# Optimization experiments

Hardware: AMD Instinct MI355X
Metric: run time of the kernel (lower is better)

The kernel has to match this reference:

```python
import jax, jax.numpy as jnp
import numpy as np

N_NODES = 50000
N_EDGES = 800000
IN_DIM = 16
HID = 128
OUT_DIM = 1
N_LAYERS = 2


def setup_inputs() -> dict:
    key = jax.random.key(0)
    ks = jax.random.split(key, 16)
    s = 0.05
    inp = {
        "edge_feats": jax.random.normal(ks[0], (N_EDGES, IN_DIM), jnp.float32),
        "node_feats": jax.random.normal(ks[1], (N_NODES, 4), jnp.float32),
        "src": jax.random.randint(ks[2], (N_EDGES,), 0, N_NODES, jnp.int32),
        "dst": jax.random.randint(ks[3], (N_EDGES,), 0, N_NODES, jnp.int32),
        # edge_embedding (dead in original forward, kept for faithfulness)
        "W_eemb": jax.random.normal(ks[4], (IN_DIM, HID), jnp.float32) * s,
        "b_eemb": jnp.zeros((HID,), jnp.float32),
        # node_embedding: Linear(4, hidden)
        "W_nemb": jax.random.normal(ks[5], (4, HID), jnp.float32) * s,
        "b_nemb": jnp.zeros((HID,), jnp.float32),
        # stacked GraphConv weights [n_layers, H, H]
        "gnn_W": jax.random.normal(ks[6], (N_LAYERS, HID, HID), jnp.float32) * s,
        "gnn_b": jnp.zeros((N_LAYERS, HID), jnp.float32),
        # output MLP
        "out_W1": jax.random.normal(ks[7], (HID, HID), jnp.float32) * s,
        "out_b1": jnp.zeros((HID,), jnp.float32),
        "out_W2": jax.random.normal(ks[8], (HID, OUT_DIM), jnp.float32) * s,
        "out_b2": jnp.zeros((OUT_DIM,), jnp.float32),
    }
    return inp


def reference(edge_feats, node_feats, src, dst, W_eemb, b_eemb, W_nemb, b_nemb,
              gnn_W, gnn_b, out_W1, out_b1, out_W2, out_b2):
    ones = jnp.ones((src.shape[0],), jnp.float32)
    deg_out = jnp.clip(jax.ops.segment_sum(ones, src, num_segments=N_NODES), 1.0)
    deg_in = jnp.clip(jax.ops.segment_sum(ones, dst, num_segments=N_NODES), 1.0)
    norm_out = deg_out ** -0.5  # [N]
    norm_in = deg_in ** -0.5    # [N]

    # edge_embedding output is dead code in the original forward (overwritten)
    _h_e = edge_feats @ W_eemb + b_eemb

    h = node_feats @ W_nemb + b_nemb  # [N, H]
    for l in range(N_LAYERS):
        # DGL GraphConv norm='both': D_out^{-1/2} gather -> scatter-sum -> D_in^{-1/2} -> W, b
        hs = h * norm_out[:, None]
        agg = jax.ops.segment_sum(hs[src], dst, num_segments=N_NODES)  # [N, H]
        h = agg * norm_in[:, None]
        h = h @ gnn_W[l] + gnn_b[l]
        h = jax.nn.relu(h)

    edge_h = h[src] + h[dst]  # apply_edges UDF, [E, H]
    x = jax.nn.relu(edge_h @ out_W1 + out_b1)
    return x @ out_W2 + out_b2  # [E, OUT_DIM]
```

## Files before the change

### kernel.cpp

```cpp
#include <hip/hip_runtime.h>

#define N_NODES 50000
#define N_EDGES 800000
#define HID 128
#define AP2 132
#define NB 256
#define NPB 196

__device__ __forceinline__ unsigned pack2bf(float a, float b) {
  unsigned ua = __float_as_uint(a);
  ua += 0x7FFFu + ((ua >> 16) & 1u);
  unsigned ub = __float_as_uint(b);
  ub += 0x7FFFu + ((ub >> 16) & 1u);
  return (ua >> 16) | (ub & 0xFFFF0000u);
}
#define BFLO(u) __uint_as_float((u) << 16)
#define BFHI(u) __uint_as_float((u) & 0xFFFF0000u)


__global__ __launch_bounds__(256) void p1_hist_kernel(
    const int* __restrict__ src, const int* __restrict__ dst,
    int* __restrict__ bcnt_d, int* __restrict__ bcnt_s) {
  __shared__ int hd[NB], hs[NB];
  int t = threadIdx.x;
  hd[t] = 0; hs[t] = 0;
  __syncthreads();
  for (int e = blockIdx.x * 256 + t; e < N_EDGES; e += gridDim.x * 256) {
    atomicAdd(&hd[dst[e] / NPB], 1);
    atomicAdd(&hs[src[e] / NPB], 1);
  }
  __syncthreads();
  if (hd[t]) atomicAdd(&bcnt_d[t], hd[t]);
  if (hs[t]) atomicAdd(&bcnt_s[t], hs[t]);
}

__global__ void p2_scan_kernel(const int* __restrict__ bcnt_d, const int* __restrict__ bcnt_s,
                               int* __restrict__ bofs_d, int* __restrict__ bofs_s,
                               int* __restrict__ cur_d, int* __restrict__ cur_s) {
  __shared__ int s[NB];
  int t = threadIdx.x;
  int v = bcnt_d[t];
  s[t] = v;
  __syncthreads();
  for (int o = 1; o < NB; o <<= 1) {
    int x = (t >= o) ? s[t - o] : 0;
    __syncthreads();
    s[t] += x;
    __syncthreads();
  }
  int ofs = s[t] - v;
  bofs_d[t] = ofs; cur_d[t] = ofs;
  if (t == NB - 1) bofs_d[NB] = s[t];
  __syncthreads();
  v = bcnt_s[t];
  s[t] = v;
  __syncthreads();
  for (int o = 1; o < NB; o <<= 1) {
    int x = (t >= o) ? s[t - o] : 0;
    __syncthreads();
    s[t] += x;
    __syncthreads();
  }
  ofs = s[t] - v;
  bofs_s[t] = ofs; cur_s[t] = ofs;
  if (t == NB - 1) bofs_s[NB] = s[t];
}

__global__ __launch_bounds__(256) void p3_scatter_dst_kernel(
    const int* __restrict__ src, const int* __restrict__ dst,
    int* __restrict__ cur_d, int2* __restrict__ sdst) {
  __shared__ int bcnt[NB], bbase[NB];
  int t = threadIdx.x;
  int base = blockIdx.x * 2048;
  bcnt[t] = 0;
  __syncthreads();
  int myb[8], myr[8], mys[8], myp[8];
#pragma unroll
  for (int u = 0; u < 8; ++u) {
    int e = base + u * 256 + t;
    myb[u] = -1;
    if (e < N_EDGES) {
      int d = dst[e];
      int b = d / NPB;
      myb[u] = b;
      myr[u] = atomicAdd(&bcnt[b], 1);
      mys[u] = src[e];
      myp[u] = ((d - b * NPB) << 20) | e;
    }
  }
  __syncthreads();
  int c = bcnt[t];
  if (c) bbase[t] = atomicAdd(&cur_d[t], c);
  __syncthreads();
#pragma unroll
  for (int u = 0; u < 8; ++u) {
    if (myb[u] >= 0) sdst[bbase[myb[u]] + myr[u]] = make_int2(mys[u], myp[u]);
  }
}

__global__ __launch_bounds__(256) void p3_scatter_src_kernel(
    const int* __restrict__ src, int* __restrict__ cur_s, int* __restrict__ ssrc) {
  __shared__ int bcnt[NB], bbase[NB];
  int t = threadIdx.x;
  int base = blockIdx.x * 2048;
  bcnt[t] = 0;
  __syncthreads();
  int myb[8], myr[8], mys[8];
#pragma unroll
  for (int u = 0; u < 8; ++u) {
    int e = base + u * 256 + t;
    myb[u] = -1;
    if (e < N_EDGES) {
      int s = src[e];
      int b = s / NPB;
      myb[u] = b;
      myr[u] = atomicAdd(&bcnt[b], 1);
      mys[u] = s;
    }
  }
  __syncthreads();
  int c = bcnt[t];
  if (c) bbase[t] = atomicAdd(&cur_s[t], c);
  __syncthreads();
#pragma unroll
  for (int u = 0; u < 8; ++u) {
    if (myb[u] >= 0) ssrc[bbase[myb[u]] + myr[u]] = mys[u];
  }
}

__global__ __launch_bounds__(256) void p4_csr_kernel(
    const int2* __restrict__ sdst, const int* __restrict__ bofs_d,
    int* __restrict__ row_ofs, float* __restrict__ norm_in,
    int* __restrict__ csr_src, int* __restrict__ csr_eid) {
  __shared__ int hc[NB], sc[NB], cur[NB];
  int b = blockIdx.x, t = threadIdx.x;
  int base = bofs_d[b], cnt = bofs_d[b + 1] - base;
  hc[t] = 0;
  __syncthreads();
  for (int i = t; i < cnt; i += 256) atomicAdd(&hc[sdst[base + i].y >> 20], 1);
  __syncthreads();
  int v = hc[t];
  sc[t] = v;
  __syncthreads();
  for (int o = 1; o < NB; o <<= 1) {
    int x = (t >= o) ? sc[t - o] : 0;
    __syncthreads();
    sc[t] += x;
    __syncthreads();
  }
  int ofs = sc[t] - v;
  int node = b * NPB + t;
  if (t < NPB && node < N_NODES) {
    row_ofs[node] = base + ofs;
    norm_in[node] = rsqrtf((float)(v < 1 ? 1 : v));
  }
  cur[t] = base + ofs;
  if (b == 0 && t == 0) row_ofs[N_NODES] = N_EDGES;
  __syncthreads();
  for (int i = t; i < cnt; i += 256) {
    int2 e = sdst[base + i];
    int pos = atomicAdd(&cur[e.y >> 20], 1);
    csr_src[pos] = e.x;
    csr_eid[pos] = e.y & 0xFFFFF;
  }
}

__global__ __launch_bounds__(256) void p5_degout_kernel(
    const int* __restrict__ ssrc, const int* __restrict__ bofs_s,
    float* __restrict__ norm_out) {
  __shared__ int hc[NB];
  int b = blockIdx.x, t = threadIdx.x;
  int base = bofs_s[b], cnt = bofs_s[b + 1] - base;
  int lo = b * NPB;
  hc[t] = 0;
  __syncthreads();
  for (int i = t; i < cnt; i += 256) atomicAdd(&hc[ssrc[base + i] - lo], 1);
  __syncthreads();
  int node = lo + t;
  if (t < NPB && node < N_NODES) {
    int v = hc[t];
    norm_out[node] = rsqrtf((float)(v < 1 ? 1 : v));
  }
}


__global__ __launch_bounds__(256) void agg4_kernel(
    const float4* __restrict__ nf4, const float* __restrict__ no_,
    const int* __restrict__ csr_src, const int* __restrict__ row_ofs,
    float4* __restrict__ agg4, float* __restrict__ sno) {
  int wid = (blockIdx.x * blockDim.x + threadIdx.x) >> 6;
  int lane = threadIdx.x & 63;
  int g = lane >> 4, l = lane & 15;
  int v = wid * 4 + g;
  if (v >= N_NODES) return;
  int beg = row_ofs[v], end = row_ofs[v + 1];
  float ax = 0.f, ay = 0.f, az = 0.f, aw = 0.f, sn = 0.f;
  for (int i = beg + l; i < end; i += 16) {
    int s = csr_src[i];
    float w = no_[s];
    float4 n = nf4[s];
    ax += n.x * w; ay += n.y * w; az += n.z * w; aw += n.w * w;
    sn += w;
  }
#pragma unroll
  for (int o = 1; o < 16; o <<= 1) {
    ax += __shfl_xor(ax, o, 16);
    ay += __shfl_xor(ay, o, 16);
    az += __shfl_xor(az, o, 16);
    aw += __shfl_xor(aw, o, 16);
    sn += __shfl_xor(sn, o, 16);
  }
  if (l == 0) {
    agg4[v] = make_float4(ax, ay, az, aw);
    sno[v] = sn;
  }
}

__global__ __launch_bounds__(256) void gemm_l1_kernel(
    const float4* __restrict__ agg4, const float* __restrict__ sno,
    const float* __restrict__ ni_, const float* __restrict__ no_,
    const float* __restrict__ Wn, const float* __restrict__ bn,
    const float* __restrict__ W0, const float* __restrict__ b0,
    uint4* __restrict__ h1b, int nrows) {
  __shared__ float At[HID * 64];
  int t = threadIdx.x;
  int v0 = blockIdx.x * 64;
  {
    int r = t & 63, kg = t >> 6;
    int v = v0 + r;
    float4 a = make_float4(0.f, 0.f, 0.f, 0.f);
    float sn = 0.f, nin = 0.f;
    if (v < nrows) { a = agg4[v]; sn = sno[v]; nin = ni_[v]; }
    for (int kk = 0; kk < 32; ++kk) {
      int k = kg * 32 + kk;
      float val = (a.x * Wn[k] + a.y * Wn[HID + k] + a.z * Wn[2 * HID + k] +
                   a.w * Wn[3 * HID + k] + bn[k] * sn) * nin;
      At[k * 64 + r] = val;
    }
  }
  __syncthreads();
  int c0 = (t >> 4) * 8, r0 = (t & 15) * 4;
  float acc[4][8];
#pragma unroll
  for (int i = 0; i < 4; ++i)
#pragma unroll
    for (int j = 0; j < 8; ++j) acc[i][j] = 0.f;

#pragma unroll 4
  for (int k = 0; k < HID; ++k) {
    float4 av = *(const float4*)&At[k * 64 + r0];
    float4 w0v = *(const float4*)&W0[k * HID + c0];
    float4 w1v = *(const float4*)&W0[k * HID + c0 + 4];
    float ar[4] = {av.x, av.y, av.z, av.w};
    float wv[8] = {w0v.x, w0v.y, w0v.z, w0v.w, w1v.x, w1v.y, w1v.z, w1v.w};
#pragma unroll
    for (int i = 0; i < 4; ++i)
#pragma unroll
      for (int j = 0; j < 8; ++j) acc[i][j] += ar[i] * wv[j];
  }
  float bb[8];
  {
    float4 b0v = *(const float4*)&b0[c0];
    float4 b1v = *(const float4*)&b0[c0 + 4];
    bb[0] = b0v.x; bb[1] = b0v.y; bb[2] = b0v.z; bb[3] = b0v.w;
    bb[4] = b1v.x; bb[5] = b1v.y; bb[6] = b1v.z; bb[7] = b1v.w;
  }
#pragma unroll
  for (int i = 0; i < 4; ++i) {
    int v = v0 + r0 + i;
    if (v < nrows) {
      float nov = no_[v];
      float o[8];
#pragma unroll
      for (int j = 0; j < 8; ++j) o[j] = fmaxf(acc[i][j] + bb[j], 0.f) * nov;
      uint4 pk;
      pk.x = pack2bf(o[0], o[1]); pk.y = pack2bf(o[2], o[3]);
      pk.z = pack2bf(o[4], o[5]); pk.w = pack2bf(o[6], o[7]);
      h1b[(size_t)v * 16 + (c0 >> 3)] = pk;
    }
  }
}

__global__ __launch_bounds__(256) void aggregate_kernel(
    const uint4* __restrict__ hb, const int* __restrict__ row_ofs,
    const int* __restrict__ csr_src, const float* __restrict__ ni_,
    float* __restrict__ agg) {
  int v = (blockIdx.x * blockDim.x + threadIdx.x) >> 6;
  int lane = threadIdx.x & 63;
  if (v >= N_NODES) return;
  int beg = row_ofs[v], end = row_ofs[v + 1];
  int g = lane >> 4, l = lane & 15;
  float acc[8];
#pragma unroll
  for (int j = 0; j < 8; ++j) acc[j] = 0.f;
  for (int i = beg; i < end; i += 16) {
    int ii[4]; float mm[4]; int ss[4];
#pragma unroll
    for (int u = 0; u < 4; ++u) {
      ii[u] = i + 4 * u + g;
      bool q = ii[u] < end;
      mm[u] = q ? 1.f : 0.f;
      ss[u] = csr_src[q ? ii[u] : beg];
    }
    uint4 X[4];
#pragma unroll
    for (int u = 0; u < 4; ++u) X[u] = hb[(size_t)ss[u] * 16 + l];
#pragma unroll
    for (int u = 0; u < 4; ++u) {
      acc[0] += BFLO(X[u].x) * mm[u]; acc[1] += BFHI(X[u].x) * mm[u];
      acc[2] += BFLO(X[u].y) * mm[u]; acc[3] += BFHI(X[u].y) * mm[u];
      acc[4] += BFLO(X[u].z) * mm[u]; acc[5] += BFHI(X[u].z) * mm[u];
      acc[6] += BFLO(X[u].w) * mm[u]; acc[7] += BFHI(X[u].w) * mm[u];
    }
  }
#pragma unroll
  for (int j = 0; j < 8; ++j) {
    acc[j] += __shfl_xor(acc[j], 16, 64);
    acc[j] += __shfl_xor(acc[j], 32, 64);
  }
  if (g == 0) {
    float n = ni_[v];
    float4 o0 = make_float4(acc[0] * n, acc[1] * n, acc[2] * n, acc[3] * n);
    float4 o1 = make_float4(acc[4] * n, acc[5] * n, acc[6] * n, acc[7] * n);
    *(float4*)&agg[(size_t)v * HID + l * 8] = o0;
    *(float4*)&agg[(size_t)v * HID + l * 8 + 4] = o1;
  }
}

__global__ __launch_bounds__(256) void gemm_dual_kernel(
    const float* __restrict__ in, const float* __restrict__ W0,
    const float* __restrict__ b0, const float* __restrict__ W1,
    uint4* __restrict__ yb, int nrows) {
  __shared__ float As[64 * AP2];
  int t = threadIdx.x;
  int v0 = blockIdx.x * 64;
  {
    const float4* in4 = (const float4*)in;
#pragma unroll
    for (int i = 0; i < 8; ++i) {
      int idx = i * 256 + t;
      int r = idx >> 5, q = idx & 31;
      int v = v0 + r;
      float4 val = make_float4(0.f, 0.f, 0.f, 0.f);
      if (v < nrows) val = in4[(size_t)v * 32 + q];
      *(float4*)&As[r * AP2 + q * 4] = val;
    }
  }
  __syncthreads();
  int c0 = (t >> 4) * 8, m = t & 15;
  float acc[4][8];
#pragma unroll
  for (int i = 0; i < 4; ++i)
#pragma unroll
    for (int j = 0; j < 8; ++j) acc[i][j] = 0.f;

#pragma unroll 4
  for (int k = 0; k < HID; ++k) {
    float4 w0v = *(const float4*)&W0[k * HID + c0];
    float4 w1v = *(const float4*)&W0[k * HID + c0 + 4];
    float ar[4];
#pragma unroll
    for (int i = 0; i < 4; ++i) ar[i] = As[(m + 16 * i) * AP2 + k];
    float wv[8] = {w0v.x, w0v.y, w0v.z, w0v.w, w1v.x, w1v.y, w1v.z, w1v.w};
#pragma unroll
    for (int i = 0; i < 4; ++i)
#pragma unroll
      for (int j = 0; j < 8; ++j) acc[i][j] += ar[i] * wv[j];
  }
  __syncthreads();
  {
    float bb[8];
    float4 b0v = *(const float4*)&b0[c0];
    float4 b1v = *(const float4*)&b0[c0 + 4];
    bb[0] = b0v.x; bb[1] = b0v.y; bb[2] = b0v.z; bb[3] = b0v.w;
    bb[4] = b1v.x; bb[5] = b1v.y; bb[6] = b1v.z; bb[7] = b1v.w;
#pragma unroll
    for (int i = 0; i < 4; ++i) {
      float4 o0, o1;
      o0.x = fmaxf(acc[i][0] + bb[0], 0.f); o0.y = fmaxf(acc[i][1] + bb[1], 0.f);
      o0.z = fmaxf(acc[i][2] + bb[2], 0.f); o0.w = fmaxf(acc[i][3] + bb[3], 0.f);
      o1.x = fmaxf(acc[i][4] + bb[4], 0.f); o1.y = fmaxf(acc[i][5] + bb[5], 0.f);
      o1.z = fmaxf(acc[i][6] + bb[6], 0.f); o1.w = fmaxf(acc[i][7] + bb[7], 0.f);
      *(float4*)&As[(m + 16 * i) * AP2 + c0] = o0;
      *(float4*)&As[(m + 16 * i) * AP2 + c0 + 4] = o1;
#pragma unroll
      for (int j = 0; j < 8; ++j) acc[i][j] = 0.f;
    }
  }
  __syncthreads();
#pragma unroll 4
  for (int k = 0; k < HID; ++k) {
    float4 w0v = *(const float4*)&W1[k * HID + c0];
    float4 w1v = *(const float4*)&W1[k * HID + c0 + 4];
    float ar[4];
#pragma unroll
    for (int i = 0; i < 4; ++i) ar[i] = As[(m + 16 * i) * AP2 + k];
    float wv[8] = {w0v.x, w0v.y, w0v.z, w0v.w, w1v.x, w1v.y, w1v.z, w1v.w};
#pragma unroll
    for (int i = 0; i < 4; ++i)
#pragma unroll
      for (int j = 0; j < 8; ++j) acc[i][j] += ar[i] * wv[j];
  }
#pragma unroll
  for (int i = 0; i < 4; ++i) {
    int v = v0 + m + 16 * i;
    if (v < nrows) {
      uint4 pk;
      pk.x = pack2bf(acc[i][0], acc[i][1]); pk.y = pack2bf(acc[i][2], acc[i][3]);
      pk.z = pack2bf(acc[i][4], acc[i][5]); pk.w = pack2bf(acc[i][6], acc[i][7]);
      yb[(size_t)v * 16 + (c0 >> 3)] = pk;
    }
  }
}

__global__ __launch_bounds__(256) void edge_out_kernel(
    const int* __restrict__ csr_src, const int* __restrict__ csr_eid,
    const int* __restrict__ row_ofs, const uint4* __restrict__ yb,
    const float* __restrict__ b1, const float* __restrict__ w2,
    const float* __restrict__ b2, float* __restrict__ out) {
  int v = (blockIdx.x * blockDim.x + threadIdx.x) >> 6;
  int lane = threadIdx.x & 63;
  if (v >= N_NODES) return;
  int beg = row_ofs[v], end = row_ofs[v + 1];
  if (beg >= end) return;
  int g = lane >> 4, l = lane & 15;
  uint4 D = yb[(size_t)v * 16 + l];
  float d[8] = {BFLO(D.x), BFHI(D.x), BFLO(D.y), BFHI(D.y),
                BFLO(D.z), BFHI(D.z), BFLO(D.w), BFHI(D.w)};
  {
    float4 q0 = ((const float4*)b1)[l * 2], q1 = ((const float4*)b1)[l * 2 + 1];
    d[0] += q0.x; d[1] += q0.y; d[2] += q0.z; d[3] += q0.w;
    d[4] += q1.x; d[5] += q1.y; d[6] += q1.z; d[7] += q1.w;
  }
  float w[8];
  {
    float4 q0 = ((const float4*)w2)[l * 2], q1 = ((const float4*)w2)[l * 2 + 1];
    w[0] = q0.x; w[1] = q0.y; w[2] = q0.z; w[3] = q0.w;
    w[4] = q1.x; w[5] = q1.y; w[6] = q1.z; w[7] = q1.w;
  }
  float ob2 = b2[0];
  for (int i = beg; i < end; i += 16) {
    int ii[4]; bool qq[4]; int ss[4];
#pragma unroll
    for (int u = 0; u < 4; ++u) {
      ii[u] = i + 4 * u + g;
      qq[u] = ii[u] < end;
      ss[u] = csr_src[qq[u] ? ii[u] : beg];
    }
    uint4 A[4];
#pragma unroll
    for (int u = 0; u < 4; ++u) A[u] = yb[(size_t)ss[u] * 16 + l];
#pragma unroll
    for (int u = 0; u < 4; ++u) {
      float p = fmaxf(BFLO(A[u].x) + d[0], 0.f) * w[0] +
                fmaxf(BFHI(A[u].x) + d[1], 0.f) * w[1] +
                fmaxf(BFLO(A[u].y) + d[2], 0.f) * w[2] +
                fmaxf(BFHI(A[u].y) + d[3], 0.f) * w[3] +
                fmaxf(BFLO(A[u].z) + d[4], 0.f) * w[4] +
                fmaxf(BFHI(A[u].z) + d[5], 0.f) * w[5] +
                fmaxf(BFLO(A[u].w) + d[6], 0.f) * w[6] +
                fmaxf(BFHI(A[u].w) + d[7], 0.f) * w[7];
      p += __shfl_down(p, 8, 16);
      p += __shfl_down(p, 4, 16);
      p += __shfl_down(p, 2, 16);
      p += __shfl_down(p, 1, 16);
      if (l == 0 && qq[u]) out[csr_eid[ii[u]]] = p + ob2;
    }
  }
}

extern "C" void kernel_launch(void* const* d_in, const int* in_sizes, int n_in,
                              void* d_out, int out_size, void* d_ws, size_t ws_size,
                              hipStream_t stream) {
  const float* node_feats = (const float*)d_in[1];
  const int*   src        = (const int*)d_in[2];
  const int*   dst        = (const int*)d_in[3];
  const float* W_nemb     = (const float*)d_in[6];
  const float* b_nemb     = (const float*)d_in[7];
  const float* gnn_W      = (const float*)d_in[8];
  const float* gnn_b      = (const float*)d_in[9];
  const float* out_W1     = (const float*)d_in[10];
  const float* out_b1     = (const float*)d_in[11];
  const float* out_W2     = (const float*)d_in[12];
  const float* out_b2     = (const float*)d_in[13];
  float* out = (float*)d_out;

  size_t off = 0;
  char* base = (char*)d_ws;
  auto alloc = [&](size_t nbytes) -> char* {
    off = (off + 255) & ~(size_t)255;
    char* p = base + off;
    off += nbytes;
    return p;
  };
  int*    bcnt2    = (int*)alloc(2 * NB * 4);
  int*    bofs_d   = (int*)alloc((NB + 1) * 4);
  int*    bofs_s   = (int*)alloc((NB + 1) * 4);
  int*    cur_d    = (int*)alloc(NB * 4);
  int*    cur_s    = (int*)alloc(NB * 4);
  float*  norm_out = (float*)alloc(N_NODES * 4);
  float*  norm_in  = (float*)alloc(N_NODES * 4);
  int*    row_ofs  = (int*)alloc((N_NODES + 1) * 4);
  int*    csr_src  = (int*)alloc((size_t)N_EDGES * 4);
  int*    csr_eid  = (int*)alloc((size_t)N_EDGES * 4);
  float4* agg4     = (float4*)alloc((size_t)N_NODES * 16);
  float*  sno      = (float*)alloc(N_NODES * 4);
  uint4*  h1b      = (uint4*)alloc((size_t)N_NODES * HID * 2);
  float*  aggbuf   = (float*)alloc((size_t)N_NODES * HID * 4);
  uint4*  yb       = (uint4*)alloc((size_t)N_NODES * HID * 2);
  int2*   sdst     = (int2*)aggbuf;
  int*    ssrc     = (int*)yb;
  int*    bcnt_d   = bcnt2;
  int*    bcnt_s   = bcnt2 + NB;
  (void)ws_size; (void)n_in; (void)in_sizes; (void)out_size;

  hipMemsetAsync(bcnt2, 0, 2 * NB * 4, stream);
  p1_hist_kernel<<<128, 256, 0, stream>>>(src, dst, bcnt_d, bcnt_s);
  p2_scan_kernel<<<1, 256, 0, stream>>>(bcnt_d, bcnt_s, bofs_d, bofs_s, cur_d, cur_s);
  p3_scatter_dst_kernel<<<(N_EDGES + 2047) / 2048, 256, 0, stream>>>(src, dst, cur_d, sdst);
  p3_scatter_src_kernel<<<(N_EDGES + 2047) / 2048, 256, 0, stream>>>(src, cur_s, ssrc);
  p4_csr_kernel<<<NB, 256, 0, stream>>>(sdst, bofs_d, row_ofs, norm_in, csr_src, csr_eid);
  p5_degout_kernel<<<NB, 256, 0, stream>>>(ssrc, bofs_s, norm_out);

  agg4_kernel<<<(N_NODES * 16 + 255) / 256, 256, 0, stream>>>(
      (const float4*)node_feats, norm_out, csr_src, row_ofs, agg4, sno);
  gemm_l1_kernel<<<(N_NODES + 63) / 64, 256, 0, stream>>>(
      agg4, sno, norm_in, norm_out, W_nemb, b_nemb, gnn_W, gnn_b, h1b, N_NODES);

  aggregate_kernel<<<(N_NODES * 64 + 255) / 256, 256, 0, stream>>>(
      h1b, row_ofs, csr_src, norm_in, aggbuf);

  gemm_dual_kernel<<<(N_NODES + 63) / 64, 256, 0, stream>>>(
      aggbuf, gnn_W + (size_t)HID * HID, gnn_b + HID, out_W1, yb, N_NODES);

  edge_out_kernel<<<(N_NODES * 64 + 255) / 256, 256, 0, stream>>>(
      csr_src, csr_eid, row_ofs, yb, out_b1, out_W2, out_b2, out);
}
```

Baseline: 361.5 us.

## Use bf16 MFMA for dual GEMM and stage layer-1 weights in LDS

Replaces the scalar FP32 dual GEMM (layer-2 GraphConv followed by the first output-MLP linear) with bf16 MFMA 16x16x32 instructions. The weights are pre-transposed and converted to bf16 by a new prep kernel. The aggregate kernel now writes bf16 instead of fp32, which halves that intermediate buffer's traffic. The layer-1 GEMM now stages W0 in shared memory in 32-row chunks instead of reading it from global memory on every k step. The cost is lower precision on the GEMM inputs and one extra small kernel launch.

Result: faster. 320.3 us (-11.4%).

```diff
diff --git a/kernel.cpp b/kernel.cpp
--- a/kernel.cpp
+++ b/kernel.cpp
@@ -3,9 +3,12 @@
 #define N_NODES 50000
 #define N_EDGES 800000
 #define HID 128
-#define AP2 132
 #define NB 256
 #define NPB 196
+#define TP 136
+
+typedef __attribute__((ext_vector_type(8))) short bf16x8;
+typedef __attribute__((ext_vector_type(4))) float f32x4;
 
 __device__ __forceinline__ unsigned pack2bf(float a, float b) {
   unsigned ua = __float_as_uint(a);
@@ -180,6 +183,17 @@
   if (t < NPB && node < N_NODES) {
     int v = hc[t];
     norm_out[node] = rsqrtf((float)(v < 1 ? 1 : v));
+  }
+}
+
+__global__ __launch_bounds__(256) void prep_w_kernel(
+    const float* __restrict__ W0, const float* __restrict__ W1,
+    short* __restrict__ Wt0, short* __restrict__ Wt1) {
+  int t = blockIdx.x * 256 + threadIdx.x;
+  if (t < HID * HID) {
+    int k = t >> 7, n = t & 127;
+    Wt0[n * HID + k] = (short)(pack2bf(W0[t], 0.f) & 0xFFFFu);
+    Wt1[n * HID + k] = (short)(pack2bf(W1[t], 0.f) & 0xFFFFu);
   }
 }
 
@@ -223,6 +237,7 @@
     const float* __restrict__ W0, const float* __restrict__ b0,
     uint4* __restrict__ h1b, int nrows) {
   __shared__ float At[HID * 64];
+  __shared__ float Wbuf[32 * HID];
   int t = threadIdx.x;
   int v0 = blockIdx.x * 64;
   {
@@ -238,7 +253,6 @@
       At[k * 64 + r] = val;
     }
   }
-  __syncthreads();
   int c0 = (t >> 4) * 8, r0 = (t & 15) * 4;
   float acc[4][8];
 #pragma unroll
@@ -246,17 +260,27 @@
 #pragma unroll
     for (int j = 0; j < 8; ++j) acc[i][j] = 0.f;
 
+  for (int kc = 0; kc < HID; kc += 32) {
+    __syncthreads();
+    {
+      const float4* wsrc = (const float4*)(W0 + kc * HID);
+      float4* wdst = (float4*)Wbuf;
+#pragma unroll
+      for (int i = 0; i < 4; ++i) wdst[i * 256 + t] = wsrc[i * 256 + t];
+    }
+    __syncthreads();
 #pragma unroll 4
-  for (int k = 0; k < HID; ++k) {
-    float4 av = *(const float4*)&At[k * 64 + r0];
-    float4 w0v = *(const float4*)&W0[k * HID + c0];
-    float4 w1v = *(const float4*)&W0[k * HID + c0 + 4];
-    float ar[4] = {av.x, av.y, av.z, av.w};
-    float wv[8] = {w0v.x, w0v.y, w0v.z, w0v.w, w1v.x, w1v.y, w1v.z, w1v.w};
-#pragma unroll
-    for (int i = 0; i < 4; ++i)
-#pragma unroll
-      for (int j = 0; j < 8; ++j) acc[i][j] += ar[i] * wv[j];
+    for (int kk = 0; kk < 32; ++kk) {
+      float4 av = *(const float4*)&At[(kc + kk) * 64 + r0];
+      float4 w0v = *(const float4*)&Wbuf[kk * HID + c0];
+      float4 w1v = *(const float4*)&Wbuf[kk * HID + c0 + 4];
+      float ar[4] = {av.x, av.y, av.z, av.w};
+      float wv[8] = {w0v.x, w0v.y, w0v.z, w0v.w, w1v.x, w1v.y, w1v.z, w1v.w};
+#pragma unroll
+      for (int i = 0; i < 4; ++i)
+#pragma unroll
+        for (int j = 0; j < 8; ++j) acc[i][j] += ar[i] * wv[j];
+    }
   }
   float bb[8];
   {
@@ -284,7 +308,7 @@
 __global__ __launch_bounds__(256) void aggregate_kernel(
     const uint4* __restrict__ hb, const int* __restrict__ row_ofs,
     const int* __restrict__ csr_src, const float* __restrict__ ni_,
-    float* __restrict__ agg) {
+    uint4* __restrict__ Ab) {
   int v = (blockIdx.x * blockDim.x + threadIdx.x) >> 6;
   int lane = threadIdx.x & 63;
   if (v >= N_NODES) return;
@@ -320,95 +344,83 @@
   }
   if (g == 0) {
     float n = ni_[v];
-    float4 o0 = make_float4(acc[0] * n, acc[1] * n, acc[2] * n, acc[3] * n);
-    float4 o1 = make_float4(acc[4] * n, acc[5] * n, acc[6] * n, acc[7] * n);
-    *(float4*)&agg[(size_t)v * HID + l * 8] = o0;
-    *(float4*)&agg[(size_t)v * HID + l * 8 + 4] = o1;
-  }
-}
-
-__global__ __launch_bounds__(256) void gemm_dual_kernel(
-    const float* __restrict__ in, const float* __restrict__ W0,
-    const float* __restrict__ b0, const float* __restrict__ W1,
-    uint4* __restrict__ yb, int nrows) {
-  __shared__ float As[64 * AP2];
+    uint4 pk;
+    pk.x = pack2bf(acc[0] * n, acc[1] * n);
+    pk.y = pack2bf(acc[2] * n, acc[3] * n);
+    pk.z = pack2bf(acc[4] * n, acc[5] * n);
+    pk.w = pack2bf(acc[6] * n, acc[7] * n);
+    Ab[(size_t)v * 16 + l] = pk;
+  }
+}
+
+__global__ __launch_bounds__(256) void gemm_dual_mfma(
+    const short* __restrict__ Ab, const short* __restrict__ Wt0,
+    const float* __restrict__ b0, const short* __restrict__ Wt1,
+    short* __restrict__ yb, int nrows) {
+  __shared__ short T1s[4][16 * TP];
   int t = threadIdx.x;
+  int w = t >> 6, lane = t & 63;
+  int m16 = lane & 15, quad = lane >> 4;
   int v0 = blockIdx.x * 64;
+  int row = v0 + w * 16 + m16;
+  bool rvalid = row < nrows;
+  int rc = rvalid ? row : (nrows - 1);
+
+  bf16x8 xfr[4];
   {
-    const float4* in4 = (const float4*)in;
-#pragma unroll
-    for (int i = 0; i < 8; ++i) {
-      int idx = i * 256 + t;
-      int r = idx >> 5, q = idx & 31;
-      int v = v0 + r;
-      float4 val = make_float4(0.f, 0.f, 0.f, 0.f);
-      if (v < nrows) val = in4[(size_t)v * 32 + q];
-      *(float4*)&As[r * AP2 + q * 4] = val;
-    }
-  }
-  __syncthreads();
-  int c0 = (t >> 4) * 8, m = t & 15;
-  float acc[4][8];
-#pragma unroll
-  for (int i = 0; i < 4; ++i)
-#pragma unroll
-    for (int j = 0; j < 8; ++j) acc[i][j] = 0.f;
-
-#pragma unroll 4
-  for (int k = 0; k < HID; ++k) {
-    float4 w0v = *(const float4*)&W0[k * HID + c0];
-    float4 w1v = *(const float4*)&W0[k * HID + c0 + 4];
-    float ar[4];
-#pragma unroll
-    for (int i = 0; i < 4; ++i) ar[i] = As[(m + 16 * i) * AP2 + k];
-    float wv[8] = {w0v.x, w0v.y, w0v.z, w0v.w, w1v.x, w1v.y, w1v.z, w1v.w};
-#pragma unroll
-    for (int i = 0; i < 4; ++i)
-#pragma unroll
-      for (int j = 0; j < 8; ++j) acc[i][j] += ar[i] * wv[j];
-  }
-  __syncthreads();
-  {
-    float bb[8];
-    float4 b0v = *(const float4*)&b0[c0];
-    float4 b1v = *(const float4*)&b0[c0 + 4];
-    bb[0] = b0v.x; bb[1] = b0v.y; bb[2] = b0v.z; bb[3] = b0v.w;
-    bb[4] = b1v.x; bb[5] = b1v.y; bb[6] = b1v.z; bb[7] = b1v.w;
-#pragma unroll
-    for (int i = 0; i < 4; ++i) {
-      float4 o0, o1;
-      o0.x = fmaxf(acc[i][0] + bb[0], 0.f); o0.y = fmaxf(acc[i][1] + bb[1], 0.f);
-      o0.z = fmaxf(acc[i][2] + bb[2], 0.f); o0.w = fmaxf(acc[i][3] + bb[3], 0.f);
-      o1.x = fmaxf(acc[i][4] + bb[4], 0.f); o1.y = fmaxf(acc[i][5] + bb[5], 0.f);
-      o1.z = fmaxf(acc[i][6] + bb[6], 0.f); o1.w = fmaxf(acc[i][7] + bb[7], 0.f);
-      *(float4*)&As[(m + 16 * i) * AP2 + c0] = o0;
-      *(float4*)&As[(m + 16 * i) * AP2 + c0 + 4] = o1;
-#pragma unroll
-      for (int j = 0; j < 8; ++j) acc[i][j] = 0.f;
-    }
-  }
-  __syncthreads();
-#pragma unroll 4
-  for (int k = 0; k < HID; ++k) {
-    float4 w0v = *(const float4*)&W1[k * HID + c0];
-    float4 w1v = *(const float4*)&W1[k * HID + c0 + 4];
-    float ar[4];
-#pragma unroll
-    for (int i = 0; i < 4; ++i) ar[i] = As[(m + 16 * i) * AP2 + k];
-    float wv[8] = {w0v.x, w0v.y, w0v.z, w0v.w, w1v.x, w1v.y, w1v.z, w1v.w};
-#pragma unroll
-    for (int i = 0; i < 4; ++i)
-#pragma unroll
-      for (int j = 0; j < 8; ++j) acc[i][j] += ar[i] * wv[j];
-  }
-#pragma unroll
-  for (int i = 0; i < 4; ++i) {
-    int v = v0 + m + 16 * i;
-    if (v < nrows) {
-      uint4 pk;
-      pk.x = pack2bf(acc[i][0], acc[i][1]); pk.y = pack2bf(acc[i][2], acc[i][3]);
-      pk.z = pack2bf(acc[i][4], acc[i][5]); pk.w = pack2bf(acc[i][6], acc[i][7]);
-      yb[(size_t)v * 16 + (c0 >> 3)] = pk;
+    const bf16x8* Ar = (const bf16x8*)(Ab + (size_t)rc * HID);
+#pragma unroll
+    for (int kc = 0; kc < 4; ++kc) xfr[kc] = Ar[kc * 4 + quad];
+  }
+  f32x4 acc[8];
+#pragma unroll
+  for (int nt = 0; nt < 8; ++nt) {
+    acc[nt][0] = 0.f; acc[nt][1] = 0.f; acc[nt][2] = 0.f; acc[nt][3] = 0.f;
+  }
+#pragma unroll
+  for (int nt = 0; nt < 8; ++nt) {
+    const bf16x8* Wr = (const bf16x8*)(Wt0 + (size_t)(nt * 16 + m16) * HID);
+#pragma unroll
+    for (int kc = 0; kc < 4; ++kc)
+      acc[nt] = __builtin_amdgcn_mfma_f32_16x16x32_bf16(Wr[kc * 4 + quad], xfr[kc],
+                                                        acc[nt], 0, 0, 0);
+  }
+  short* T1w = &T1s[w][0];
+#pragma unroll
+  for (int nt = 0; nt < 8; ++nt) {
+    int nb = nt * 16 + quad * 4;
+    float4 bv = *(const float4*)&b0[nb];
+    float r0 = fmaxf(acc[nt][0] + bv.x, 0.f);
+    float r1 = fmaxf(acc[nt][1] + bv.y, 0.f);
+    float r2 = fmaxf(acc[nt][2] + bv.z, 0.f);
+    float r3 = fmaxf(acc[nt][3] + bv.w, 0.f);
+    uint2 pk;
+    pk.x = pack2bf(r0, r1);
+    pk.y = pack2bf(r2, r3);
+    *(uint2*)&T1w[m16 * TP + nb] = pk;
+    acc[nt][0] = 0.f; acc[nt][1] = 0.f; acc[nt][2] = 0.f; acc[nt][3] = 0.f;
+  }
+  __syncthreads();
+  bf16x8 tfr[4];
+#pragma unroll
+  for (int kc = 0; kc < 4; ++kc)
+    tfr[kc] = *(const bf16x8*)&T1w[m16 * TP + kc * 32 + quad * 8];
+#pragma unroll
+  for (int nt = 0; nt < 8; ++nt) {
+    const bf16x8* Wr = (const bf16x8*)(Wt1 + (size_t)(nt * 16 + m16) * HID);
+#pragma unroll
+    for (int kc = 0; kc < 4; ++kc)
+      acc[nt] = __builtin_amdgcn_mfma_f32_16x16x32_bf16(Wr[kc * 4 + quad], tfr[kc],
+                                                        acc[nt], 0, 0, 0);
+  }
+  if (rvalid) {
+#pragma unroll
+    for (int nt = 0; nt < 8; ++nt) {
+      int nb = nt * 16 + quad * 4;
+      uint2 pk;
+      pk.x = pack2bf(acc[nt][0], acc[nt][1]);
+      pk.y = pack2bf(acc[nt][2], acc[nt][3]);
+      *(uint2*)(yb + (size_t)row * HID + nb) = pk;
     }
   }
 }
@@ -505,16 +517,20 @@
   int*    csr_eid  = (int*)alloc((size_t)N_EDGES * 4);
   float4* agg4     = (float4*)alloc((size_t)N_NODES * 16);
   float*  sno      = (float*)alloc(N_NODES * 4);
+  short*  Wt0      = (short*)alloc((size_t)HID * HID * 2);
+  short*  Wt1      = (short*)alloc((size_t)HID * HID * 2);
   uint4*  h1b      = (uint4*)alloc((size_t)N_NODES * HID * 2);
-  float*  aggbuf   = (float*)alloc((size_t)N_NODES * HID * 4);
-  uint4*  yb       = (uint4*)alloc((size_t)N_NODES * HID * 2);
-  int2*   sdst     = (int2*)aggbuf;
-  int*    ssrc     = (int*)yb;
+  short*  Ab       = (short*)alloc((size_t)N_NODES * HID * 2);
+  short*  ybs      = (short*)alloc((size_t)N_NODES * HID * 2);
+  int2*   sdst     = (int2*)Ab;
+  int*    ssrc     = (int*)ybs;
   int*    bcnt_d   = bcnt2;
   int*    bcnt_s   = bcnt2 + NB;
   (void)ws_size; (void)n_in; (void)in_sizes; (void)out_size;
 
   hipMemsetAsync(bcnt2, 0, 2 * NB * 4, stream);
+  prep_w_kernel<<<(HID * HID + 255) / 256, 256, 0, stream>>>(
+      gnn_W + (size_t)HID * HID, out_W1, Wt0, Wt1);
   p1_hist_kernel<<<128, 256, 0, stream>>>(src, dst, bcnt_d, bcnt_s);
   p2_scan_kernel<<<1, 256, 0, stream>>>(bcnt_d, bcnt_s, bofs_d, bofs_s, cur_d, cur_s);
   p3_scatter_dst_kernel<<<(N_EDGES + 2047) / 2048, 256, 0, stream>>>(src, dst, cur_d, sdst);
@@ -528,11 +544,11 @@
       agg4, sno, norm_in, norm_out, W_nemb, b_nemb, gnn_W, gnn_b, h1b, N_NODES);
 
   aggregate_kernel<<<(N_NODES * 64 + 255) / 256, 256, 0, stream>>>(
-      h1b, row_ofs, csr_src, norm_in, aggbuf);
-
-  gemm_dual_kernel<<<(N_NODES + 63) / 64, 256, 0, stream>>>(
-      aggbuf, gnn_W + (size_t)HID * HID, gnn_b + HID, out_W1, yb, N_NODES);
+      h1b, row_ofs, csr_src, norm_in, (uint4*)Ab);
+
+  gemm_dual_mfma<<<(N_NODES + 63) / 64, 256, 0, stream>>>(
+      Ab, Wt0, gnn_b + HID, Wt1, ybs, N_NODES);
 
   edge_out_kernel<<<(N_NODES * 64 + 255) / 256, 256, 0, stream>>>(
-      csr_src, csr_eid, row_ofs, yb, out_b1, out_W2, out_b2, out);
-}
+      csr_src, csr_eid, row_ofs, (const uint4*)ybs, out_b1, out_W2, out_b2, out);
+}
```
